# Kernel optimization log

Hardware: AMD Instinct MI355X
Metric: run time of the kernel (lower is better)

Reference implementation:

```python
import jax, jax.numpy as jnp
import numpy as np

K_HEADS = 8
D_HEAD = 8
C_IN = 128   # c_x + c_t after channel concat
C_OUT = K_HEADS * D_HEAD  # 64
SMALL = -32767.0  # -2**15 + 1


def setup_inputs() -> dict:
    key = jax.random.key(0)
    ks = jax.random.split(key, 12)
    B, Cx, V, T = 8, 64, 200, 128
    x = jax.random.normal(ks[0], (B, Cx, V, T), dtype=jnp.float32)
    tem_embedding = jax.random.normal(ks[1], (B, Cx, V, T), dtype=jnp.float32)
    s = 0.05
    Wq = jax.random.normal(ks[2], (C_OUT, C_IN), dtype=jnp.float32) * s
    bq = jax.random.normal(ks[3], (C_OUT,), dtype=jnp.float32) * s
    Wk = jax.random.normal(ks[4], (C_OUT, C_IN), dtype=jnp.float32) * s
    bk = jax.random.normal(ks[5], (C_OUT,), dtype=jnp.float32) * s
    Wv = jax.random.normal(ks[6], (C_OUT, C_IN), dtype=jnp.float32) * s
    bv = jax.random.normal(ks[7], (C_OUT,), dtype=jnp.float32) * s
    Wo = jax.random.normal(ks[8], (C_OUT, C_OUT), dtype=jnp.float32) * s
    bo = jax.random.normal(ks[9], (C_OUT,), dtype=jnp.float32) * s
    return {"x": x, "tem_embedding": tem_embedding,
            "Wq": Wq, "bq": bq, "Wk": Wk, "bk": bk,
            "Wv": Wv, "bv": bv, "Wo": Wo, "bo": bo}


def reference(x, tem_embedding, Wq, bq, Wk, bk, Wv, bv, Wo, bo):
    B, _, V, T = x.shape
    # concat temporal embedding on channel dim (last T steps)
    xt = jnp.concatenate([x, tem_embedding[:, :, :, -T:]], axis=1)  # [B, C_IN, V, T]

    def proj(W, b):  # 1x1 conv == channel einsum
        return jnp.einsum('oi,bivt->bovt', W, xt) + b[None, :, None, None]

    def heads(t):  # [B, K*d, V, T] -> [K*B, V, T, d] (split on dim1, cat on dim0)
        t = t.reshape(B, K_HEADS, D_HEAD, V, T)
        t = jnp.transpose(t, (1, 0, 3, 4, 2))  # [K, B, V, T, d]
        return t.reshape(K_HEADS * B, V, T, D_HEAD)

    q = heads(proj(Wq, bq))
    k = heads(proj(Wk, bk))
    v = heads(proj(Wv, bv))

    attn = jnp.einsum('nvtd,nvsd->nvts', q, k) / jnp.sqrt(jnp.float32(D_HEAD))
    causal = jnp.tril(jnp.ones((T, T), dtype=bool))  # [T, T]
    attn = jnp.where(causal[None, None, :, :], attn, SMALL)
    attn = jax.nn.softmax(attn, axis=-1)
    out = jnp.einsum('nvts,nvsd->nvtd', attn, v)  # [K*B, V, T, d]

    # merge heads back: [K*B, V, T, d] -> [B, K*d, V, T]
    out = out.reshape(K_HEADS, B, V, T, D_HEAD)
    out = jnp.transpose(out, (1, 0, 4, 2, 3)).reshape(B, K_HEADS * D_HEAD, V, T)
    out = jnp.einsum('oi,bivt->bovt', Wo, out) + bo[None, :, None, None]
    return jax.nn.relu(out)
```

## Files before the change

kernel.cpp:

```cpp
#include <hip/hip_runtime.h>
#include <stdint.h>

#define TPB 512

constexpr int Bb   = 8;
constexpr int Vv   = 200;
constexpr int Tt   = 128;
constexpr int CIN  = 128;
constexpr int COUT = 64;

typedef __attribute__((ext_vector_type(8))) short bf16x8;
typedef __attribute__((ext_vector_type(4))) short short4v;
typedef __attribute__((ext_vector_type(4))) float f32x4;

__device__ __forceinline__ unsigned short f2bf(float f) {
    union { float f; unsigned u; } x; x.f = f;
    unsigned r = x.u + 0x7fffu + ((x.u >> 16) & 1u);
    return (unsigned short)(r >> 16);
}
__device__ __forceinline__ unsigned pk2(float a, float b) {
    return (unsigned)f2bf(a) | ((unsigned)f2bf(b) << 16);
}

#if __has_builtin(__builtin_amdgcn_mfma_f32_16x16x16bf16_1k)
#define MFMA16(a, b, c) __builtin_amdgcn_mfma_f32_16x16x16bf16_1k(a, b, c, 0, 0, 0)
#else
__device__ __forceinline__ f32x4 mfma16_asm(short4v a, short4v b, f32x4 c) {
    f32x4 d;
    asm("v_mfma_f32_16x16x16_bf16 %0, %1, %2, %3" : "=v"(d) : "v"(a), "v"(b), "v"(c));
    return d;
}
#define MFMA16(a, b, c) mfma16_asm(a, b, c)
#endif

__global__ void prep_w(const float* __restrict__ Wq, const float* __restrict__ Wk,
                       const float* __restrict__ Wv, const float* __restrict__ Wo,
                       unsigned short* __restrict__ ws) {
    int i = blockIdx.x * 256 + threadIdx.x;
    float v;
    if (i < 8192)       v = Wq[i];
    else if (i < 16384) v = Wk[i - 8192];
    else if (i < 24576) v = Wv[i - 16384];
    else                v = Wo[i - 24576];
    ws[i] = f2bf(v);
}

__global__ __launch_bounds__(TPB, 6)
void tatt_fused(const float* __restrict__ x, const float* __restrict__ tem,
                const float* __restrict__ bq, const float* __restrict__ bk,
                const float* __restrict__ bv, const float* __restrict__ bo,
                const unsigned short* __restrict__ ws,
                float* __restrict__ out)
{
    __shared__ __align__(16) unsigned char smem[53248];
    unsigned short* qk = (unsigned short*)smem;
    unsigned short* vt = (unsigned short*)(smem + 32768);
    unsigned short* ot = (unsigned short*)(smem + 32768);
    unsigned short* xt = (unsigned short*)(smem + 49152);

    const int tid = threadIdx.x;
    const int w = tid >> 6, lane = tid & 63;
    const int l15 = lane & 15, qd = lane >> 4;
    const int b = blockIdx.x / Vv, v = blockIdx.x % Vv;
    const float QS = 1.44269504088896f * 0.35355339059327f;

    {
        const int tl = tid & 15, cq = tid >> 4;
        const int c0 = cq * 4;
        const float* sbase = (c0 < 64 ? x : tem)
            + ((b * 64 + (c0 & 63)) * Vv + v) * Tt + tl;
        constexpr int CS = Vv * Tt;
        float c0v = sbase[0], c1v = sbase[CS], c2v = sbase[2 * CS], c3v = sbase[3 * CS];
        const int xoff = tl * CIN + ((((c0 >> 3) ^ tl) << 3) + (c0 & 7));

        auto tile_mfma = [&](int tile, int r) {
            const int p = tile >> 2, ot_ = tile & 3;
            f32x4 acc = {0.f, 0.f, 0.f, 0.f};
            const unsigned short* Wb  = ws + p * 8192 + (ot_ * 16 + l15) * CIN + qd * 8;
            const unsigned short* Bbp = xt + l15 * CIN;
            #pragma unroll
            for (int kc = 0; kc < 4; ++kc) {
                bf16x8 a = *(const bf16x8*)(Wb + kc * 32);
                int phys = (kc * 4 + qd) ^ l15;
                bf16x8 bbv = *(const bf16x8*)(Bbp + phys * 8);
                acc = __builtin_amdgcn_mfma_f32_16x16x32_bf16(a, bbv, acc, 0, 0, 0);
            }
            const int obase = ot_ * 16 + qd * 4;
            const float* bp = (p == 0) ? bq : (p == 1 ? bk : bv);
            float4 bias = *(const float4*)(bp + obase);
            float bb4[4] = {bias.x, bias.y, bias.z, bias.w};
            const int tg = r * 16 + l15;
            if (p == 2) {
                #pragma unroll
                for (int rr = 0; rr < 4; ++rr) {
                    int dg = obase + rr;
                    int tp = tg ^ ((((dg >> 2) & 3)) << 4);
                    vt[dg * 128 + tp] = f2bf(acc[rr] + bb4[rr]);
                }
            } else {
                float sc = (p == 0) ? QS : 1.0f;
                ushort4 s4;
                s4.x = f2bf((acc[0] + bb4[0]) * sc);
                s4.y = f2bf((acc[1] + bb4[1]) * sc);
                s4.z = f2bf((acc[2] + bb4[2]) * sc);
                s4.w = f2bf((acc[3] + bb4[3]) * sc);
                int phys = (obase >> 2) ^ (tg & 14);
                *(ushort4*)(qk + p * 8192 + tg * 64 + phys * 4) = s4;
            }
        };

        for (int r = 0; r < 8; ++r) {
            if (r) __syncthreads();
            ushort4 s4;
            s4.x = f2bf(c0v); s4.y = f2bf(c1v); s4.z = f2bf(c2v); s4.w = f2bf(c3v);
            *(ushort4*)(xt + xoff) = s4;
            if (r < 7) {
                int o = (r + 1) * 16;
                c0v = sbase[o];          c1v = sbase[CS + o];
                c2v = sbase[2 * CS + o]; c3v = sbase[3 * CS + o];
            }
            __syncthreads();
            const int wr = (w + ((r & 1) << 2)) & 7;
            tile_mfma(wr, r);
            if (wr < 4) tile_mfma(8 + wr, r);
        }
    }
    __syncthreads();

    {
        const int h = w;
        short4v vfrag[8];
        {
            const int dg = h * 8 + l15;
            const int swz = ((dg >> 2) & 3) << 4;
            #pragma unroll
            for (int st = 0; st < 8; ++st) {
                short4v f = {0, 0, 0, 0};
                if (l15 < 8) {
                    int sp = (st * 16 + qd * 4) ^ swz;
                    f = *(const short4v*)(vt + dg * 128 + sp);
                }
                vfrag[st] = f;
            }
        }
        __syncthreads();

        bool dmask[4];
        #pragma unroll
        for (int r = 0; r < 4; ++r) dmask[r] = (qd * 4 + r) <= l15;
        const int qkoff = ((h * 2 + qd) ^ (l15 & 14)) << 2;

        for (int tt = 0; tt < 8; ++tt) {
            short4v qf = {0, 0, 0, 0};
            if (qd < 2) qf = *(const short4v*)(qk + (tt * 16 + l15) * 64 + qkoff);
            f32x4 o0 = {0.f, 0.f, 0.f, 0.f}, o1 = {0.f, 0.f, 0.f, 0.f};
            float lac = 0.f;
            #pragma unroll
            for (int st = 0; st < 8; ++st) {
                if (st <= tt) {
                    short4v kf = {0, 0, 0, 0};
                    if (qd < 2) kf = *(const short4v*)(qk + 8192 + (st * 16 + l15) * 64 + qkoff);
                    f32x4 z = {0.f, 0.f, 0.f, 0.f};
                    f32x4 s = MFMA16(kf, qf, z);
                    float p0 = __builtin_amdgcn_exp2f(s[0]);
                    float p1 = __builtin_amdgcn_exp2f(s[1]);
                    float p2 = __builtin_amdgcn_exp2f(s[2]);
                    float p3 = __builtin_amdgcn_exp2f(s[3]);
                    if (st == tt) {
                        p0 = dmask[0] ? p0 : 0.f;
                        p1 = dmask[1] ? p1 : 0.f;
                        p2 = dmask[2] ? p2 : 0.f;
                        p3 = dmask[3] ? p3 : 0.f;
                    }
                    lac += (p0 + p1) + (p2 + p3);
                    int pp0 = (int)pk2(p0, p1), pp1 = (int)pk2(p2, p3);
                    short4v pf;
                    pf[0] = (short)(pp0 & 0xffff); pf[1] = (short)(pp0 >> 16);
                    pf[2] = (short)(pp1 & 0xffff); pf[3] = (short)(pp1 >> 16);
                    if (st & 1) o1 = MFMA16(vfrag[st], pf, o1);
                    else        o0 = MFMA16(vfrag[st], pf, o0);
                }
            }
            float l = lac;
            l += __shfl_xor(l, 16, 64);
            l += __shfl_xor(l, 32, 64);
            float rl = __builtin_amdgcn_rcpf(l);
            if (qd < 2) {
                float r0 = (o0[0] + o1[0]) * rl, r1 = (o0[1] + o1[1]) * rl;
                float r2 = (o0[2] + o1[2]) * rl, r3 = (o0[3] + o1[3]) * rl;
                int t = tt * 16 + l15;
                uint2 st2;
                st2.x = pk2(r0, r1);
                st2.y = pk2(r2, r3);
                *(uint2*)(ot + t * 64 + (((h * 2 + qd) ^ (l15 & 14)) << 2)) = st2;
            }
        }
    }
    __syncthreads();

    {
        const int tt = w;
        #pragma unroll
        for (int ot_ = 0; ot_ < 4; ++ot_) {
            f32x4 acc = {0.f, 0.f, 0.f, 0.f};
            const unsigned short* Ab = ws + 24576 + (ot_ * 16 + l15) * COUT + qd * 8;
            #pragma unroll
            for (int kc = 0; kc < 2; ++kc) {
                bf16x8 a = *(const bf16x8*)(Ab + kc * 32);
                bf16x8 bbv = *(const bf16x8*)(ot + (tt * 16 + l15) * 64
                                 + (((kc * 8 + qd * 2) ^ (l15 & 14)) << 2));
                acc = __builtin_amdgcn_mfma_f32_16x16x32_bf16(a, bbv, acc, 0, 0, 0);
            }
            int obase = ot_ * 16 + qd * 4;
            float4 bias = *(const float4*)(bo + obase);
            float bb4[4] = {bias.x, bias.y, bias.z, bias.w};
            int t = tt * 16 + l15;
            #pragma unroll
            for (int r = 0; r < 4; ++r) {
                float val = acc[r] + bb4[r];
                out[((b * COUT + obase + r) * Vv + v) * Tt + t] = val > 0.f ? val : 0.f;
            }
        }
    }
}

extern "C" void kernel_launch(void* const* d_in, const int* in_sizes, int n_in,
                              void* d_out, int out_size, void* d_ws, size_t ws_size,
                              hipStream_t stream) {
    (void)in_sizes; (void)n_in; (void)ws_size; (void)out_size;
    const float* x   = (const float*)d_in[0];
    const float* tem = (const float*)d_in[1];
    const float* Wq  = (const float*)d_in[2];
    const float* bq  = (const float*)d_in[3];
    const float* Wk  = (const float*)d_in[4];
    const float* bk  = (const float*)d_in[5];
    const float* Wv  = (const float*)d_in[6];
    const float* bv  = (const float*)d_in[7];
    const float* Wo  = (const float*)d_in[8];
    const float* bo  = (const float*)d_in[9];
    float* out = (float*)d_out;
    unsigned short* ws = (unsigned short*)d_ws;

    prep_w<<<dim3(112), dim3(256), 0, stream>>>(Wq, Wk, Wv, Wo, ws);
    tatt_fused<<<dim3(Bb * Vv), dim3(TPB), 0, stream>>>(
        x, tem, bq, bk, bv, bo, ws, out);
}
```

Before: 252.1 us.

## Hold weight fragments in registers, drop the weight prep kernel, vectorize input loads

Removes the separate fp32-to-bf16 weight conversion kernel. Each wave now loads and converts its own Q/K/V weight fragments once into registers before the projection loop. The work split is fixed: waves 0-3 compute the Q and K tiles and waves 4-7 compute V. Input staging switches from strided scalar loads to float4 loads along time with scalar LDS stores, the attention loop is fully unrolled, and the output projection reuses per-wave Wo fragments across two time tiles. This cuts one launch and repeated global weight reads, at the cost of more register pressure and redundant per-block conversion work.

```diff
diff --git a/kernel.cpp b/kernel.cpp
--- a/kernel.cpp
+++ b/kernel.cpp
@@ -33,23 +33,12 @@
 #define MFMA16(a, b, c) mfma16_asm(a, b, c)
 #endif
 
-__global__ void prep_w(const float* __restrict__ Wq, const float* __restrict__ Wk,
-                       const float* __restrict__ Wv, const float* __restrict__ Wo,
-                       unsigned short* __restrict__ ws) {
-    int i = blockIdx.x * 256 + threadIdx.x;
-    float v;
-    if (i < 8192)       v = Wq[i];
-    else if (i < 16384) v = Wk[i - 8192];
-    else if (i < 24576) v = Wv[i - 16384];
-    else                v = Wo[i - 24576];
-    ws[i] = f2bf(v);
-}
-
 __global__ __launch_bounds__(TPB, 6)
 void tatt_fused(const float* __restrict__ x, const float* __restrict__ tem,
-                const float* __restrict__ bq, const float* __restrict__ bk,
-                const float* __restrict__ bv, const float* __restrict__ bo,
-                const unsigned short* __restrict__ ws,
+                const float* __restrict__ Wq, const float* __restrict__ bq,
+                const float* __restrict__ Wk, const float* __restrict__ bk,
+                const float* __restrict__ Wv, const float* __restrict__ bv,
+                const float* __restrict__ Wo, const float* __restrict__ bo,
                 float* __restrict__ out)
 {
     __shared__ __align__(16) unsigned char smem[53248];
@@ -64,65 +53,88 @@
     const int b = blockIdx.x / Vv, v = blockIdx.x % Vv;
     const float QS = 1.44269504088896f * 0.35355339059327f;
 
-    {
-        const int tl = tid & 15, cq = tid >> 4;
-        const int c0 = cq * 4;
-        const float* sbase = (c0 < 64 ? x : tem)
-            + ((b * 64 + (c0 & 63)) * Vv + v) * Tt + tl;
-        constexpr int CS = Vv * Tt;
-        float c0v = sbase[0], c1v = sbase[CS], c2v = sbase[2 * CS], c3v = sbase[3 * CS];
-        const int xoff = tl * CIN + ((((c0 >> 3) ^ tl) << 3) + (c0 & 7));
-
-        auto tile_mfma = [&](int tile, int r) {
-            const int p = tile >> 2, ot_ = tile & 3;
-            f32x4 acc = {0.f, 0.f, 0.f, 0.f};
-            const unsigned short* Wb  = ws + p * 8192 + (ot_ * 16 + l15) * CIN + qd * 8;
-            const unsigned short* Bbp = xt + l15 * CIN;
+    bf16x8 afr0[4], afr1[4];
+    {
+        const float* W0 = (w < 4) ? Wq : Wv;
+        const int o0_ = (w < 4) ? w : (w - 4);
+        const float* base0 = W0 + (o0_ * 16 + l15) * CIN + qd * 8;
+        #pragma unroll
+        for (int kc = 0; kc < 4; ++kc) {
+            float4 fa = *(const float4*)(base0 + kc * 32);
+            float4 fb = *(const float4*)(base0 + kc * 32 + 4);
+            union { bf16x8 v8; unsigned u[4]; } t;
+            t.u[0] = pk2(fa.x, fa.y); t.u[1] = pk2(fa.z, fa.w);
+            t.u[2] = pk2(fb.x, fb.y); t.u[3] = pk2(fb.z, fb.w);
+            afr0[kc] = t.v8;
+        }
+        if (w < 4) {
+            const float* base1 = Wk + (w * 16 + l15) * CIN + qd * 8;
             #pragma unroll
             for (int kc = 0; kc < 4; ++kc) {
-                bf16x8 a = *(const bf16x8*)(Wb + kc * 32);
-                int phys = (kc * 4 + qd) ^ l15;
-                bf16x8 bbv = *(const bf16x8*)(Bbp + phys * 8);
-                acc = __builtin_amdgcn_mfma_f32_16x16x32_bf16(a, bbv, acc, 0, 0, 0);
-            }
-            const int obase = ot_ * 16 + qd * 4;
-            const float* bp = (p == 0) ? bq : (p == 1 ? bk : bv);
-            float4 bias = *(const float4*)(bp + obase);
-            float bb4[4] = {bias.x, bias.y, bias.z, bias.w};
-            const int tg = r * 16 + l15;
-            if (p == 2) {
-                #pragma unroll
-                for (int rr = 0; rr < 4; ++rr) {
-                    int dg = obase + rr;
-                    int tp = tg ^ ((((dg >> 2) & 3)) << 4);
-                    vt[dg * 128 + tp] = f2bf(acc[rr] + bb4[rr]);
-                }
-            } else {
-                float sc = (p == 0) ? QS : 1.0f;
-                ushort4 s4;
-                s4.x = f2bf((acc[0] + bb4[0]) * sc);
-                s4.y = f2bf((acc[1] + bb4[1]) * sc);
-                s4.z = f2bf((acc[2] + bb4[2]) * sc);
-                s4.w = f2bf((acc[3] + bb4[3]) * sc);
-                int phys = (obase >> 2) ^ (tg & 14);
-                *(ushort4*)(qk + p * 8192 + tg * 64 + phys * 4) = s4;
-            }
-        };
+                float4 fa = *(const float4*)(base1 + kc * 32);
+                float4 fb = *(const float4*)(base1 + kc * 32 + 4);
+                union { bf16x8 v8; unsigned u[4]; } t;
+                t.u[0] = pk2(fa.x, fa.y); t.u[1] = pk2(fa.z, fa.w);
+                t.u[2] = pk2(fb.x, fb.y); t.u[3] = pk2(fb.z, fb.w);
+                afr1[kc] = t.v8;
+            }
+        }
+    }
+
+    auto tileC = [&](const bf16x8 (&A)[4], int p, int ot_, int r) {
+        f32x4 acc = {0.f, 0.f, 0.f, 0.f};
+        const unsigned short* Bbp = xt + l15 * CIN;
+        #pragma unroll
+        for (int kc = 0; kc < 4; ++kc) {
+            int phys = (kc * 4 + qd) ^ l15;
+            bf16x8 bb = *(const bf16x8*)(Bbp + phys * 8);
+            acc = __builtin_amdgcn_mfma_f32_16x16x32_bf16(A[kc], bb, acc, 0, 0, 0);
+        }
+        const int obase = ot_ * 16 + qd * 4;
+        const float* bp = (p == 0) ? bq : ((p == 1) ? bk : bv);
+        float4 bias = *(const float4*)(bp + obase);
+        float bb4[4] = {bias.x, bias.y, bias.z, bias.w};
+        const int tg = r * 16 + l15;
+        if (p == 2) {
+            #pragma unroll
+            for (int rr = 0; rr < 4; ++rr) {
+                int dg = obase + rr;
+                int tp = tg ^ ((((dg >> 2) & 3)) << 4);
+                vt[dg * 128 + tp] = f2bf(acc[rr] + bb4[rr]);
+            }
+        } else {
+            float sc = (p == 0) ? QS : 1.0f;
+            ushort4 s4;
+            s4.x = f2bf((acc[0] + bb4[0]) * sc);
+            s4.y = f2bf((acc[1] + bb4[1]) * sc);
+            s4.z = f2bf((acc[2] + bb4[2]) * sc);
+            s4.w = f2bf((acc[3] + bb4[3]) * sc);
+            int phys = (obase >> 2) ^ (tg & 14);
+            *(ushort4*)(qk + p * 8192 + tg * 64 + phys * 4) = s4;
+        }
+    };
+
+    {
+        const int sc_ = tid >> 2;
+        const int stq = tid & 3;
+        const float* sbase = (sc_ < 64 ? x : tem)
+            + ((b * 64 + (sc_ & 63)) * Vv + v) * Tt + stq * 4;
+        float4 pf = *(const float4*)(sbase);
+        const int clow = sc_ & 7, chi = sc_ >> 3;
 
         for (int r = 0; r < 8; ++r) {
             if (r) __syncthreads();
-            ushort4 s4;
-            s4.x = f2bf(c0v); s4.y = f2bf(c1v); s4.z = f2bf(c2v); s4.w = f2bf(c3v);
-            *(ushort4*)(xt + xoff) = s4;
-            if (r < 7) {
-                int o = (r + 1) * 16;
-                c0v = sbase[o];          c1v = sbase[CS + o];
-                c2v = sbase[2 * CS + o]; c3v = sbase[3 * CS + o];
-            }
+            {
+                int t0 = stq * 4;
+                xt[(t0 + 0) * CIN + ((chi ^ (t0 + 0)) << 3) + clow] = f2bf(pf.x);
+                xt[(t0 + 1) * CIN + ((chi ^ (t0 + 1)) << 3) + clow] = f2bf(pf.y);
+                xt[(t0 + 2) * CIN + ((chi ^ (t0 + 2)) << 3) + clow] = f2bf(pf.z);
+                xt[(t0 + 3) * CIN + ((chi ^ (t0 + 3)) << 3) + clow] = f2bf(pf.w);
+            }
+            if (r < 7) pf = *(const float4*)(sbase + (r + 1) * 16);
             __syncthreads();
-            const int wr = (w + ((r & 1) << 2)) & 7;
-            tile_mfma(wr, r);
-            if (wr < 4) tile_mfma(8 + wr, r);
+            if (w < 4) { tileC(afr0, 0, w, r); tileC(afr1, 1, w, r); }
+            else       { tileC(afr0, 2, w - 4, r); }
         }
     }
     __syncthreads();
@@ -150,6 +162,7 @@
         for (int r = 0; r < 4; ++r) dmask[r] = (qd * 4 + r) <= l15;
         const int qkoff = ((h * 2 + qd) ^ (l15 & 14)) << 2;
 
+        #pragma unroll
         for (int tt = 0; tt < 8; ++tt) {
             short4v qf = {0, 0, 0, 0};
             if (qd < 2) qf = *(const short4v*)(qk + (tt * 16 + l15) * 64 + qkoff);
@@ -199,26 +212,44 @@
     __syncthreads();
 
     {
-        const int tt = w;
-        #pragma unroll
-        for (int ot_ = 0; ot_ < 4; ++ot_) {
-            f32x4 acc = {0.f, 0.f, 0.f, 0.f};
-            const unsigned short* Ab = ws + 24576 + (ot_ * 16 + l15) * COUT + qd * 8;
+        const int tq3 = w & 3, ohB = (w >> 2) * 2;
+        bf16x8 wof[2][2];
+        #pragma unroll
+        for (int oth = 0; oth < 2; ++oth) {
+            const float* base = Wo + ((ohB + oth) * 16 + l15) * COUT + qd * 8;
             #pragma unroll
             for (int kc = 0; kc < 2; ++kc) {
-                bf16x8 a = *(const bf16x8*)(Ab + kc * 32);
-                bf16x8 bbv = *(const bf16x8*)(ot + (tt * 16 + l15) * 64
-                                 + (((kc * 8 + qd * 2) ^ (l15 & 14)) << 2));
-                acc = __builtin_amdgcn_mfma_f32_16x16x32_bf16(a, bbv, acc, 0, 0, 0);
-            }
-            int obase = ot_ * 16 + qd * 4;
-            float4 bias = *(const float4*)(bo + obase);
-            float bb4[4] = {bias.x, bias.y, bias.z, bias.w};
-            int t = tt * 16 + l15;
-            #pragma unroll
-            for (int r = 0; r < 4; ++r) {
-                float val = acc[r] + bb4[r];
-                out[((b * COUT + obase + r) * Vv + v) * Tt + t] = val > 0.f ? val : 0.f;
+                float4 fa = *(const float4*)(base + kc * 32);
+                float4 fb = *(const float4*)(base + kc * 32 + 4);
+                union { bf16x8 v8; unsigned u[4]; } t;
+                t.u[0] = pk2(fa.x, fa.y); t.u[1] = pk2(fa.z, fa.w);
+                t.u[2] = pk2(fb.x, fb.y); t.u[3] = pk2(fb.z, fb.w);
+                wof[oth][kc] = t.v8;
+            }
+        }
+        #pragma unroll
+        for (int ts = 0; ts < 2; ++ts) {
+            const int tt = tq3 * 2 + ts;
+            #pragma unroll
+            for (int oth = 0; oth < 2; ++oth) {
+                const int ot_ = ohB + oth;
+                f32x4 acc = {0.f, 0.f, 0.f, 0.f};
+                #pragma unroll
+                for (int kc = 0; kc < 2; ++kc) {
+                    bf16x8 bb = *(const bf16x8*)(ot + (tt * 16 + l15) * 64
+                                     + (((kc * 8 + qd * 2) ^ (l15 & 14)) << 2));
+                    acc = __builtin_amdgcn_mfma_f32_16x16x32_bf16(wof[oth][kc], bb, acc, 0, 0, 0);
+                }
+                const int obase = ot_ * 16 + qd * 4;
+                float4 bias = *(const float4*)(bo + obase);
+                const int t = tt * 16 + l15;
+                float vr[4] = {acc[0] + bias.x, acc[1] + bias.y,
+                               acc[2] + bias.z, acc[3] + bias.w};
+                #pragma unroll
+                for (int r = 0; r < 4; ++r) {
+                    float val = vr[r];
+                    out[((b * COUT + obase + r) * Vv + v) * Tt + t] = val > 0.f ? val : 0.f;
+                }
             }
         }
     }
@@ -227,7 +258,7 @@
 extern "C" void kernel_launch(void* const* d_in, const int* in_sizes, int n_in,
                               void* d_out, int out_size, void* d_ws, size_t ws_size,
                               hipStream_t stream) {
-    (void)in_sizes; (void)n_in; (void)ws_size; (void)out_size;
+    (void)in_sizes; (void)n_in; (void)ws_size; (void)out_size; (void)d_ws;
     const float* x   = (const float*)d_in[0];
     const float* tem = (const float*)d_in[1];
     const float* Wq  = (const float*)d_in[2];
@@ -239,9 +270,7 @@
     const float* Wo  = (const float*)d_in[8];
     const float* bo  = (const float*)d_in[9];
     float* out = (float*)d_out;
-    unsigned short* ws = (unsigned short*)d_ws;
-
-    prep_w<<<dim3(112), dim3(256), 0, stream>>>(Wq, Wk, Wv, Wo, ws);
+
     tatt_fused<<<dim3(Bb * Vv), dim3(TPB), 0, stream>>>(
-        x, tem, bq, bk, bv, bo, ws, out);
-}
+        x, tem, Wq, bq, Wk, bk, Wv, bv, Wo, bo, out);
+}
```

New measurement: 224.4 us. 11.0% less time.
